# Optimization experiments

Measured on AMD Instinct MI355X. Metric: run time of the kernel, lower is better.

## Reference

```python
import jax, jax.numpy as jnp
import numpy as np

EPS = 1e-5
N_LAYERS_TOTAL = 4  # n_layers + 1 convs


def setup_inputs() -> dict:
    key = jax.random.key(0)
    ks = jax.random.split(key, 6)
    B, N, C = 16, 2048, 128
    x = jax.random.normal(ks[0], (B, N, C), dtype=jnp.float32)
    adj = jax.random.uniform(ks[1], (B, N, N), dtype=jnp.float32)
    # per-layer params: weight [L,Cin,Cout], bias [L,Cout], bn gamma/beta [L,C]
    W = jax.random.normal(ks[2], (N_LAYERS_TOTAL, C, C), dtype=jnp.float32) * (1.0 / np.sqrt(C))
    b = jnp.zeros((N_LAYERS_TOTAL, C), dtype=jnp.float32)
    gamma = jnp.ones((N_LAYERS_TOTAL, C), dtype=jnp.float32)
    beta = jnp.zeros((N_LAYERS_TOTAL, C), dtype=jnp.float32)
    return {"x": x, "adj": adj, "W": W, "b": b, "gamma": gamma, "beta": beta}


def reference(x, adj, W, b, gamma, beta):
    # Stacked dense GCNConv -> ReLU -> BatchNorm1d (training mode).
    h = x
    for i in range(N_LAYERS_TOTAL):
        # GCNConv (dense, normalize=False): adj @ (h @ W) + b
        h = jnp.einsum('bnm,bmc->bnc', adj, h @ W[i]) + b[i]  # [B,N,C]
        h = jax.nn.relu(h)
        # BatchNorm over flattened (B*N) per channel, biased variance
        mu = jnp.mean(h, axis=(0, 1))
        var = jnp.mean(jnp.square(h - mu), axis=(0, 1))
        h = gamma[i] * (h - mu) * jax.lax.rsqrt(var + EPS) + beta[i]
    return h
```

## Files before the change

kernel.cpp:

```cpp
#include <hip/hip_runtime.h>
#include <stdint.h>
#include <stddef.h>

#define BATCH 16
#define NROW 2048
#define CH 128
#define NLAYER 4
#define NN_TOT (BATCH * NROW)
#define EPSV 1e-5f

typedef short short8 __attribute__((ext_vector_type(8)));
typedef float f32x4 __attribute__((ext_vector_type(4)));

static __device__ __forceinline__ unsigned short f2bf(float f) {
  union { float f; unsigned int i; } v;
  v.f = f;
  unsigned int u = v.i;
  return (unsigned short)((u + 0x7FFFu + ((u >> 16) & 1u)) >> 16);
}
static __device__ __forceinline__ short8 pack8(const float* __restrict__ p) {
  f32x4 a = *(const f32x4*)p;
  f32x4 b = *(const f32x4*)(p + 4);
  short8 v;
  v[0] = (short)f2bf(a[0]); v[1] = (short)f2bf(a[1]);
  v[2] = (short)f2bf(a[2]); v[3] = (short)f2bf(a[3]);
  v[4] = (short)f2bf(b[0]); v[5] = (short)f2bf(b[1]);
  v[6] = (short)f2bf(b[2]); v[7] = (short)f2bf(b[3]);
  return v;
}

__global__ __launch_bounds__(256) void cvt_kernel(
    const float* __restrict__ src, unsigned short* __restrict__ dst) {
  const int n8 = BATCH * NROW * NROW / 8;
  for (int i = blockIdx.x * blockDim.x + threadIdx.x; i < n8;
       i += gridDim.x * blockDim.x) {
    *(short8*)(dst + (size_t)i * 8) = pack8(src + (size_t)i * 8);
  }
}

__global__ void prep_kernel(const float* __restrict__ Wl,
                            const float* __restrict__ gprev,
                            const float* __restrict__ bprev,
                            float* __restrict__ gsum, float* __restrict__ gsumsq,
                            unsigned short* __restrict__ Wt,
                            float* __restrict__ cvec,
                            float* __restrict__ sg, float* __restrict__ tg,
                            int first, int do_fold) {
  __shared__ float ss[CH], tt[CH];
  const int t = threadIdx.x;
  float s_, t_;
  if (first) {
    s_ = 1.0f; t_ = 0.0f;
  } else {
    const float inv = 1.0f / (float)NN_TOT;
    float mu = gsum[t] * inv;
    float var = gsumsq[t] * inv - mu * mu;
    s_ = gprev[t] * rsqrtf(var + EPSV);
    t_ = bprev[t] - mu * s_;
  }
  ss[t] = s_; tt[t] = t_;
  sg[t] = s_; tg[t] = t_;
  gsum[t] = 0.0f; gsumsq[t] = 0.0f;
  __syncthreads();
  if (do_fold) {
    float acc = 0.0f;
    for (int c = 0; c < CH; ++c) {
      float w = Wl[c * CH + t];
      acc += tt[c] * w;
      Wt[t * CH + c] = f2bf(ss[c] * w);
    }
    cvec[t] = acc;
  }
}

__global__ __launch_bounds__(256) void gemm1_kernel(
    const float* __restrict__ X,
    const unsigned short* __restrict__ Wt,
    const float* __restrict__ cvec,
    unsigned short* __restrict__ Yt) {
  __shared__ unsigned short As[64 * 128];
  __shared__ unsigned short Bs[128 * 128];
  const int tid = threadIdx.x;
  const int m0 = blockIdx.x * 64;

#pragma unroll
  for (int j = 0; j < 4; ++j) {
    int c = tid + 256 * j;
    int r = c >> 4, slot = c & 15;
    int kc = slot ^ (r & 15);
    *(short8*)(As + c * 8) = pack8(X + (size_t)(m0 + r) * CH + kc * 8);
  }
#pragma unroll
  for (int j = 0; j < 8; ++j) {
    int c = tid + 256 * j;
    int r = c >> 4, slot = c & 15;
    int kc = slot ^ (r & 15);
    *(short8*)(Bs + c * 8) = *(const short8*)(Wt + (size_t)r * CH + kc * 8);
  }
  __syncthreads();

  const int l = tid & 63, w = tid >> 6;
  const int mq = (w >> 1) * 32, oq = (w & 1) * 64;
  const int lr = l & 15, lq = l >> 4;
  f32x4 acc[2][4] = {};

#pragma unroll
  for (int kt = 0; kt < 4; ++kt) {
    const int kc0 = kt * 4 + lq;
    const int slotK = kc0 ^ lr;
    short8 a[2], b[4];
#pragma unroll
    for (int mi = 0; mi < 2; ++mi)
      a[mi] = *(const short8*)(As + (mq + mi * 16 + lr) * 128 + slotK * 8);
#pragma unroll
    for (int ni = 0; ni < 4; ++ni)
      b[ni] = *(const short8*)(Bs + (oq + ni * 16 + lr) * 128 + slotK * 8);
#pragma unroll
    for (int mi = 0; mi < 2; ++mi)
#pragma unroll
      for (int ni = 0; ni < 4; ++ni)
        acc[mi][ni] = __builtin_amdgcn_mfma_f32_16x16x32_bf16(a[mi], b[ni], acc[mi][ni], 0, 0, 0);
  }

  const int bat = m0 >> 11;
  const int mb = m0 & 2047;
  unsigned short* YtB = Yt + (size_t)bat * CH * NROW;
#pragma unroll
  for (int ni = 0; ni < 4; ++ni) {
    const int o = oq + ni * 16 + lr;
    const float cv = cvec[o];
    unsigned short* row = YtB + (size_t)o * NROW;
#pragma unroll
    for (int mi = 0; mi < 2; ++mi) {
      const int m = mb + mq + mi * 16 + lq * 4;
      f32x4 v = acc[mi][ni];
      unsigned short p0 = f2bf(v[0] + cv), p1 = f2bf(v[1] + cv);
      unsigned short p2 = f2bf(v[2] + cv), p3 = f2bf(v[3] + cv);
      unsigned long long packed = (unsigned long long)p0 | ((unsigned long long)p1 << 16) |
                                  ((unsigned long long)p2 << 32) | ((unsigned long long)p3 << 48);
      *(unsigned long long*)(row + m) = packed;
    }
  }
}

__global__ __launch_bounds__(256) void gemm2_kernel(
    const unsigned short* __restrict__ adjb,
    const unsigned short* __restrict__ Yt,
    const float* __restrict__ bias,
    float* __restrict__ R,
    float* __restrict__ gsum, float* __restrict__ gsumsq) {
  __shared__ unsigned short As[128 * 32];
  __shared__ unsigned short Bs[64 * 32];
  __shared__ float redS[2][CH];
  __shared__ float redQ[2][CH];
  const int tid = threadIdx.x;
  const int bat = blockIdx.x >> 5;
  const int n0 = (blockIdx.x & 31) * 64;
  const unsigned short* adjB = adjb + (size_t)bat * NROW * NROW;
  const unsigned short* YtB = Yt + (size_t)bat * CH * NROW;

  const int rA = tid >> 2;
  const int kcS = (tid & 3) ^ ((rA >> 1) & 3);
  const unsigned short* gA0 = YtB + (size_t)rA * NROW + kcS * 8;
  const unsigned short* gA1 = gA0 + (size_t)64 * NROW;
  const unsigned short* gB0 = adjB + (size_t)(n0 + rA) * NROW + kcS * 8;
  unsigned short* lA0 = As + tid * 8;
  unsigned short* lA1 = As + 2048 + tid * 8;
  unsigned short* lB0 = Bs + tid * 8;

  const int l = tid & 63, w = tid >> 6;
  const int cq = (w >> 1) * 64;
  const int nh = (w & 1) * 32;
  const int lr = l & 15, lq = l >> 4;
  const int slotL = lq ^ ((lr >> 1) & 3);
  const int aoff = (cq + lr) * 32 + slotL * 8;
  const int boff = (nh + lr) * 32 + slotL * 8;

  f32x4 acc[4][2] = {};

  short8 pa0 = *(const short8*)gA0;
  short8 pa1 = *(const short8*)gA1;
  short8 pb0 = *(const short8*)gB0;

  for (int kt = 0; kt < 64; ++kt) {
    __syncthreads();
    *(short8*)lA0 = pa0;
    *(short8*)lA1 = pa1;
    *(short8*)lB0 = pb0;
    __syncthreads();
    if (kt < 63) {
      const int k0 = (kt + 1) * 32;
      pa0 = *(const short8*)(gA0 + k0);
      pa1 = *(const short8*)(gA1 + k0);
      pb0 = *(const short8*)(gB0 + k0);
    }
    short8 a[4], b[2];
#pragma unroll
    for (int mi = 0; mi < 4; ++mi) a[mi] = *(const short8*)(As + aoff + mi * 512);
#pragma unroll
    for (int ni = 0; ni < 2; ++ni) b[ni] = *(const short8*)(Bs + boff + ni * 512);
#pragma unroll
    for (int mi = 0; mi < 4; ++mi)
#pragma unroll
      for (int ni = 0; ni < 2; ++ni)
        acc[mi][ni] = __builtin_amdgcn_mfma_f32_16x16x32_bf16(a[mi], b[ni], acc[mi][ni], 0, 0, 0);
  }

  float* RB = R + (size_t)bat * NROW * CH;
  f32x4 sumv[4] = {};
  f32x4 sumq[4] = {};
#pragma unroll
  for (int mi = 0; mi < 4; ++mi) {
    const int c0 = cq + mi * 16 + lq * 4;
    f32x4 bia = *(const f32x4*)(bias + c0);
#pragma unroll
    for (int ni = 0; ni < 2; ++ni) {
      const int n = n0 + nh + ni * 16 + lr;
      f32x4 v = acc[mi][ni] + bia;
      v[0] = fmaxf(v[0], 0.0f);
      v[1] = fmaxf(v[1], 0.0f);
      v[2] = fmaxf(v[2], 0.0f);
      v[3] = fmaxf(v[3], 0.0f);
      sumv[mi] += v;
      sumq[mi] += v * v;
      *(f32x4*)(RB + (size_t)n * CH + c0) = v;
    }
  }
#pragma unroll
  for (int mi = 0; mi < 4; ++mi) {
#pragma unroll
    for (int d = 1; d < 16; d <<= 1) {
      sumv[mi][0] += __shfl_xor(sumv[mi][0], d);
      sumv[mi][1] += __shfl_xor(sumv[mi][1], d);
      sumv[mi][2] += __shfl_xor(sumv[mi][2], d);
      sumv[mi][3] += __shfl_xor(sumv[mi][3], d);
      sumq[mi][0] += __shfl_xor(sumq[mi][0], d);
      sumq[mi][1] += __shfl_xor(sumq[mi][1], d);
      sumq[mi][2] += __shfl_xor(sumq[mi][2], d);
      sumq[mi][3] += __shfl_xor(sumq[mi][3], d);
    }
  }
  const int nqi = w & 1;
  if (lr == 0) {
#pragma unroll
    for (int mi = 0; mi < 4; ++mi) {
      const int c0 = cq + mi * 16 + lq * 4;
      redS[nqi][c0 + 0] = sumv[mi][0];
      redS[nqi][c0 + 1] = sumv[mi][1];
      redS[nqi][c0 + 2] = sumv[mi][2];
      redS[nqi][c0 + 3] = sumv[mi][3];
      redQ[nqi][c0 + 0] = sumq[mi][0];
      redQ[nqi][c0 + 1] = sumq[mi][1];
      redQ[nqi][c0 + 2] = sumq[mi][2];
      redQ[nqi][c0 + 3] = sumq[mi][3];
    }
  }
  __syncthreads();
  if (tid < CH) {
    atomicAdd(gsum + tid, redS[0][tid] + redS[1][tid]);
  } else {
    const int c = tid - CH;
    atomicAdd(gsumsq + c, redQ[0][c] + redQ[1][c]);
  }
}

__global__ void out_kernel(float* __restrict__ out,
                           const float* __restrict__ sg,
                           const float* __restrict__ tg) {
  const int total = NN_TOT * CH / 4;
  for (int idx = blockIdx.x * blockDim.x + threadIdx.x; idx < total;
       idx += gridDim.x * blockDim.x) {
    f32x4 v = *(f32x4*)(out + (size_t)idx * 4);
    const int c0 = (idx & 31) * 4;
    f32x4 s = *(const f32x4*)(sg + c0);
    f32x4 t = *(const f32x4*)(tg + c0);
    v = s * v + t;
    *(f32x4*)(out + (size_t)idx * 4) = v;
  }
}

extern "C" void kernel_launch(void* const* d_in, const int* in_sizes, int n_in,
                              void* d_out, int out_size, void* d_ws, size_t ws_size,
                              hipStream_t stream) {
  (void)in_sizes; (void)n_in; (void)out_size; (void)ws_size;
  const float* x     = (const float*)d_in[0];
  const float* adj   = (const float*)d_in[1];
  const float* W     = (const float*)d_in[2];
  const float* bvec  = (const float*)d_in[3];
  const float* gamma = (const float*)d_in[4];
  const float* beta  = (const float*)d_in[5];

  float* R = (float*)d_out;

  char* ws = (char*)d_ws;
  unsigned short* adjb = (unsigned short*)(ws);
  unsigned short* Yt   = (unsigned short*)(ws + 134217728);
  unsigned short* Wt   = (unsigned short*)(ws + 142606336);
  float* cvec   = (float*)(ws + 142606336 + 32768);
  float* sg     = (float*)(ws + 142606336 + 33280);
  float* tg     = (float*)(ws + 142606336 + 33792);
  float* gsum   = (float*)(ws + 142606336 + 34304);
  float* gsumsq = (float*)(ws + 142606336 + 34816);

  cvt_kernel<<<8192, 256, 0, stream>>>(adj, adjb);

  for (int i = 0; i < NLAYER; ++i) {
    prep_kernel<<<1, 128, 0, stream>>>(
        W + (size_t)i * CH * CH,
        gamma + (size_t)(i ? (i - 1) : 0) * CH, beta + (size_t)(i ? (i - 1) : 0) * CH,
        gsum, gsumsq, Wt, cvec, sg, tg, (i == 0) ? 1 : 0, 1);
    gemm1_kernel<<<512, 256, 0, stream>>>((i == 0) ? x : R, Wt, cvec, Yt);
    gemm2_kernel<<<512, 256, 0, stream>>>(adjb, Yt, bvec + (size_t)i * CH, R,
                                          gsum, gsumsq);
  }
  prep_kernel<<<1, 128, 0, stream>>>(W, gamma + 3 * CH, beta + 3 * CH,
                                     gsum, gsumsq, Wt, cvec, sg, tg, 0, 0);
  out_kernel<<<512, 256, 0, stream>>>(R, sg, tg);
}
```

Baseline: 718.9 us.

## Fuse adj bf16 conversion into first GEMM2 and double-buffer LDS with K=64 tiles

Removes the separate adjacency fp32-to-bf16 conversion kernel. The first layer's aggregation GEMM now reads fp32 adj, converts it in registers, feeds it to the MFMA tiles and writes the bf16 copy for later layers. The aggregation GEMM also moves to a 64-wide K tile with double-buffered LDS and two stages of register prefetch, using one barrier per tile. This saves a full extra read pass over the adjacency matrix and cuts barrier count, at the cost of more LDS and register pressure, which may lower occupancy.

```diff
diff --git a/kernel.cpp b/kernel.cpp
--- a/kernel.cpp
+++ b/kernel.cpp
@@ -8,6 +8,8 @@
 #define NLAYER 4
 #define NN_TOT (BATCH * NROW)
 #define EPSV 1e-5f
+#define KS 64
+#define NKT (NROW / KS)
 
 typedef short short8 __attribute__((ext_vector_type(8)));
 typedef float f32x4 __attribute__((ext_vector_type(4)));
@@ -27,15 +29,6 @@
   v[4] = (short)f2bf(b[0]); v[5] = (short)f2bf(b[1]);
   v[6] = (short)f2bf(b[2]); v[7] = (short)f2bf(b[3]);
   return v;
-}
-
-__global__ __launch_bounds__(256) void cvt_kernel(
-    const float* __restrict__ src, unsigned short* __restrict__ dst) {
-  const int n8 = BATCH * NROW * NROW / 8;
-  for (int i = blockIdx.x * blockDim.x + threadIdx.x; i < n8;
-       i += gridDim.x * blockDim.x) {
-    *(short8*)(dst + (size_t)i * 8) = pack8(src + (size_t)i * 8);
-  }
 }
 
 __global__ void prep_kernel(const float* __restrict__ Wl,
@@ -143,68 +136,158 @@
   }
 }
 
+struct Pf {
+  short8 a0, a1, a2, a3;
+  short8 b0, b1;
+  f32x4 f0, f1, f2, f3;
+};
+
+template <int CVT>
 __global__ __launch_bounds__(256) void gemm2_kernel(
-    const unsigned short* __restrict__ adjb,
+    const float* __restrict__ adjF,
+    const unsigned short* __restrict__ adjH,
+    unsigned short* __restrict__ adjO,
     const unsigned short* __restrict__ Yt,
     const float* __restrict__ bias,
     float* __restrict__ R,
     float* __restrict__ gsum, float* __restrict__ gsumsq) {
-  __shared__ unsigned short As[128 * 32];
-  __shared__ unsigned short Bs[64 * 32];
+  __shared__ unsigned short As[2][CH * KS];
+  __shared__ unsigned short Bs[2][64 * KS];
   __shared__ float redS[2][CH];
   __shared__ float redQ[2][CH];
+
   const int tid = threadIdx.x;
   const int bat = blockIdx.x >> 5;
   const int n0 = (blockIdx.x & 31) * 64;
-  const unsigned short* adjB = adjb + (size_t)bat * NROW * NROW;
   const unsigned short* YtB = Yt + (size_t)bat * CH * NROW;
 
-  const int rA = tid >> 2;
-  const int kcS = (tid & 3) ^ ((rA >> 1) & 3);
-  const unsigned short* gA0 = YtB + (size_t)rA * NROW + kcS * 8;
-  const unsigned short* gA1 = gA0 + (size_t)64 * NROW;
-  const unsigned short* gB0 = adjB + (size_t)(n0 + rA) * NROW + kcS * 8;
-  unsigned short* lA0 = As + tid * 8;
-  unsigned short* lA1 = As + 2048 + tid * 8;
-  unsigned short* lB0 = Bs + tid * 8;
+  const int s8 = tid & 7;
+  const int r8 = tid >> 3;
+  const int swz8 = (s8 ^ (r8 & 7)) * 8;
+
+  const unsigned short* gA0 = YtB + (size_t)r8 * NROW + s8 * 8;
+  const unsigned short* gA1 = gA0 + (size_t)32 * NROW;
+  const unsigned short* gA2 = gA0 + (size_t)64 * NROW;
+  const unsigned short* gA3 = gA0 + (size_t)96 * NROW;
+  const int lA0 = r8 * KS + swz8;
+  const int lA1 = lA0 + 32 * KS;
+  const int lA2 = lA0 + 64 * KS;
+  const int lA3 = lA0 + 96 * KS;
+
+  const size_t bO0 = (size_t)bat * NROW * NROW + (size_t)(n0 + r8) * NROW + s8 * 8;
+  const size_t bO1 = bO0 + (size_t)32 * NROW;
+  const int lB0 = r8 * KS + swz8;
+  const int lB1 = lB0 + 32 * KS;
 
   const int l = tid & 63, w = tid >> 6;
   const int cq = (w >> 1) * 64;
   const int nh = (w & 1) * 32;
   const int lr = l & 15, lq = l >> 4;
-  const int slotL = lq ^ ((lr >> 1) & 3);
-  const int aoff = (cq + lr) * 32 + slotL * 8;
-  const int boff = (nh + lr) * 32 + slotL * 8;
+  const int rsw = lr & 7;
 
   f32x4 acc[4][2] = {};
 
-  short8 pa0 = *(const short8*)gA0;
-  short8 pa1 = *(const short8*)gA1;
-  short8 pb0 = *(const short8*)gB0;
-
-  for (int kt = 0; kt < 64; ++kt) {
-    __syncthreads();
-    *(short8*)lA0 = pa0;
-    *(short8*)lA1 = pa1;
-    *(short8*)lB0 = pb0;
-    __syncthreads();
-    if (kt < 63) {
-      const int k0 = (kt + 1) * 32;
-      pa0 = *(const short8*)(gA0 + k0);
-      pa1 = *(const short8*)(gA1 + k0);
-      pb0 = *(const short8*)(gB0 + k0);
-    }
-    short8 a[4], b[2];
-#pragma unroll
-    for (int mi = 0; mi < 4; ++mi) a[mi] = *(const short8*)(As + aoff + mi * 512);
-#pragma unroll
-    for (int ni = 0; ni < 2; ++ni) b[ni] = *(const short8*)(Bs + boff + ni * 512);
-#pragma unroll
-    for (int mi = 0; mi < 4; ++mi)
-#pragma unroll
-      for (int ni = 0; ni < 2; ++ni)
-        acc[mi][ni] = __builtin_amdgcn_mfma_f32_16x16x32_bf16(a[mi], b[ni], acc[mi][ni], 0, 0, 0);
-  }
+  auto LOADS = [&](Pf& p, int kt) {
+    const int k0 = kt * KS;
+    p.a0 = *(const short8*)(gA0 + k0);
+    p.a1 = *(const short8*)(gA1 + k0);
+    p.a2 = *(const short8*)(gA2 + k0);
+    p.a3 = *(const short8*)(gA3 + k0);
+    if constexpr (CVT) {
+      const float* q0 = adjF + bO0 + k0;
+      const float* q1 = adjF + bO1 + k0;
+      p.f0 = *(const f32x4*)q0; p.f1 = *(const f32x4*)(q0 + 4);
+      p.f2 = *(const f32x4*)q1; p.f3 = *(const f32x4*)(q1 + 4);
+    } else {
+      p.b0 = *(const short8*)(adjH + bO0 + k0);
+      p.b1 = *(const short8*)(adjH + bO1 + k0);
+    }
+  };
+
+  auto WRITES = [&](Pf& p, int buf, int kt) {
+    unsigned short* Ap = As[buf];
+    *(short8*)(Ap + lA0) = p.a0;
+    *(short8*)(Ap + lA1) = p.a1;
+    *(short8*)(Ap + lA2) = p.a2;
+    *(short8*)(Ap + lA3) = p.a3;
+    unsigned short* Bp = Bs[buf];
+    if constexpr (CVT) {
+      short8 q0, q1;
+      q0[0] = (short)f2bf(p.f0[0]); q0[1] = (short)f2bf(p.f0[1]);
+      q0[2] = (short)f2bf(p.f0[2]); q0[3] = (short)f2bf(p.f0[3]);
+      q0[4] = (short)f2bf(p.f1[0]); q0[5] = (short)f2bf(p.f1[1]);
+      q0[6] = (short)f2bf(p.f1[2]); q0[7] = (short)f2bf(p.f1[3]);
+      q1[0] = (short)f2bf(p.f2[0]); q1[1] = (short)f2bf(p.f2[1]);
+      q1[2] = (short)f2bf(p.f2[2]); q1[3] = (short)f2bf(p.f2[3]);
+      q1[4] = (short)f2bf(p.f3[0]); q1[5] = (short)f2bf(p.f3[1]);
+      q1[6] = (short)f2bf(p.f3[2]); q1[7] = (short)f2bf(p.f3[3]);
+      *(short8*)(Bp + lB0) = q0;
+      *(short8*)(Bp + lB1) = q1;
+      const int k0 = kt * KS;
+      *(short8*)(adjO + bO0 + k0) = q0;
+      *(short8*)(adjO + bO1 + k0) = q1;
+    } else {
+      *(short8*)(Bp + lB0) = p.b0;
+      *(short8*)(Bp + lB1) = p.b1;
+    }
+  };
+
+  auto COMPUTE = [&](int buf) {
+    const unsigned short* Ap = As[buf];
+    const unsigned short* Bp = Bs[buf];
+#pragma unroll
+    for (int ks = 0; ks < 2; ++ks) {
+      const int sl = ((ks * 4 + lq) ^ rsw) * 8;
+      short8 a0 = *(const short8*)(Ap + (cq +  0 + lr) * KS + sl);
+      short8 a1 = *(const short8*)(Ap + (cq + 16 + lr) * KS + sl);
+      short8 a2 = *(const short8*)(Ap + (cq + 32 + lr) * KS + sl);
+      short8 a3 = *(const short8*)(Ap + (cq + 48 + lr) * KS + sl);
+      short8 b0 = *(const short8*)(Bp + (nh +  0 + lr) * KS + sl);
+      short8 b1 = *(const short8*)(Bp + (nh + 16 + lr) * KS + sl);
+      acc[0][0] = __builtin_amdgcn_mfma_f32_16x16x32_bf16(a0, b0, acc[0][0], 0, 0, 0);
+      acc[0][1] = __builtin_amdgcn_mfma_f32_16x16x32_bf16(a0, b1, acc[0][1], 0, 0, 0);
+      acc[1][0] = __builtin_amdgcn_mfma_f32_16x16x32_bf16(a1, b0, acc[1][0], 0, 0, 0);
+      acc[1][1] = __builtin_amdgcn_mfma_f32_16x16x32_bf16(a1, b1, acc[1][1], 0, 0, 0);
+      acc[2][0] = __builtin_amdgcn_mfma_f32_16x16x32_bf16(a2, b0, acc[2][0], 0, 0, 0);
+      acc[2][1] = __builtin_amdgcn_mfma_f32_16x16x32_bf16(a2, b1, acc[2][1], 0, 0, 0);
+      acc[3][0] = __builtin_amdgcn_mfma_f32_16x16x32_bf16(a3, b0, acc[3][0], 0, 0, 0);
+      acc[3][1] = __builtin_amdgcn_mfma_f32_16x16x32_bf16(a3, b1, acc[3][1], 0, 0, 0);
+    }
+  };
+
+#define BAR() do { asm volatile("s_waitcnt lgkmcnt(0)"); __builtin_amdgcn_s_barrier(); } while (0)
+
+  Pf s0, s1;
+  LOADS(s0, 0);
+  WRITES(s0, 0, 0);
+  LOADS(s0, 1);
+  LOADS(s1, 2);
+  BAR();
+
+#pragma unroll 1
+  for (int kt2 = 0; kt2 < 14; ++kt2) {
+    const int kt = kt2 * 2;
+    COMPUTE(0);
+    WRITES(s0, 1, kt + 1);
+    LOADS(s0, kt + 3);
+    BAR();
+    COMPUTE(1);
+    WRITES(s1, 0, kt + 2);
+    LOADS(s1, kt + 4);
+    BAR();
+  }
+  COMPUTE(0);
+  WRITES(s0, 1, 29);
+  LOADS(s0, 31);
+  BAR();
+  COMPUTE(1);
+  WRITES(s1, 0, 30);
+  BAR();
+  COMPUTE(0);
+  WRITES(s0, 1, 31);
+  BAR();
+  COMPUTE(1);
+#undef BAR
 
   float* RB = R + (size_t)bat * NROW * CH;
   f32x4 sumv[4] = {};
@@ -302,16 +385,20 @@
   float* gsum   = (float*)(ws + 142606336 + 34304);
   float* gsumsq = (float*)(ws + 142606336 + 34816);
 
-  cvt_kernel<<<8192, 256, 0, stream>>>(adj, adjb);
-
   for (int i = 0; i < NLAYER; ++i) {
     prep_kernel<<<1, 128, 0, stream>>>(
         W + (size_t)i * CH * CH,
         gamma + (size_t)(i ? (i - 1) : 0) * CH, beta + (size_t)(i ? (i - 1) : 0) * CH,
         gsum, gsumsq, Wt, cvec, sg, tg, (i == 0) ? 1 : 0, 1);
     gemm1_kernel<<<512, 256, 0, stream>>>((i == 0) ? x : R, Wt, cvec, Yt);
-    gemm2_kernel<<<512, 256, 0, stream>>>(adjb, Yt, bvec + (size_t)i * CH, R,
-                                          gsum, gsumsq);
+    if (i == 0) {
+      gemm2_kernel<1><<<512, 256, 0, stream>>>(adj, nullptr, adjb, Yt,
+                                               bvec, R, gsum, gsumsq);
+    } else {
+      gemm2_kernel<0><<<512, 256, 0, stream>>>(nullptr, adjb, nullptr, Yt,
+                                               bvec + (size_t)i * CH, R,
+                                               gsum, gsumsq);
+    }
   }
   prep_kernel<<<1, 128, 0, stream>>>(W, gamma + 3 * CH, beta + 3 * CH,
                                      gsum, gsumsq, Wt, cvec, sg, tg, 0, 0);
```

New measurement: 648.9 us. -9.7%, faster.
